# Performance work log

Hardware: AMD Instinct MI355X
Metric: run time of the kernel (lower is better)

The kernel has to match this reference:

```python
import jax, jax.numpy as jnp
import numpy as np


def squash(s, axis=-1):
    sq = jnp.sum(s * s, axis=axis, keepdims=True)
    return sq / (1.0 + sq) * s / (jnp.sqrt(sq) + 1e-8)


def setup_inputs() -> dict:
    key = jax.random.key(0)
    k1, k2 = jax.random.split(key)
    B, IN_CAPS, IN_DIM = 32, 2048, 16
    NUM_CAPS, CAPS_DIM = 32, 32
    x = jax.random.normal(k1, (B, IN_CAPS, IN_DIM), dtype=jnp.float32)
    W = 0.01 * jax.random.normal(k2, (NUM_CAPS, IN_CAPS, CAPS_DIM, IN_DIM), dtype=jnp.float32)
    return {"x": x, "W": W, "routing_steps": 3}


def reference(x, W, routing_steps):
    # u_hat[b, j, i, c] = W[j, i, c, d] @ x[b, i, d]
    u_hat = jnp.einsum('jicd,bid->bjic', W, x)
    du = jax.lax.stop_gradient(u_hat)  # routing uses detached predictions
    B, J, I, C = u_hat.shape
    b = jnp.zeros((B, J, I, 1), dtype=u_hat.dtype)
    for _ in range(routing_steps - 1):
        c = jax.nn.softmax(b, axis=1)                  # over output capsules j
        s = jnp.sum(c * du, axis=2)                    # [B, J, C]
        v = squash(s)
        b = b + jnp.einsum('bjic,bjc->bji', du, v)[..., None]
    c = jax.nn.softmax(b, axis=1)
    s = jnp.sum(c * u_hat, axis=2)
    v = squash(s)                                      # [B, J, C]
    return v
```

## Files before the change

### kernel.cpp

```cpp
#include <hip/hip_runtime.h>
#include <hip/hip_bf16.h>

#define B_SZ   32
#define I_CAPS 2048
#define J_CAPS 32
#define C_DIM  32
#define D_DIM  16

#define IT     8
#define TILES  8
#define SPLIT  32
#define MPAD   72

typedef _Float16 f16x8 __attribute__((ext_vector_type(8)));
typedef _Float16 f16x4 __attribute__((ext_vector_type(4)));
typedef float    f32x4 __attribute__((ext_vector_type(4)));

__device__ __forceinline__ float h2f_lo(unsigned int p) {
    union { unsigned short s; _Float16 h; } cv; cv.s = (unsigned short)(p & 0xffffu);
    return (float)cv.h;
}
__device__ __forceinline__ float h2f_hi(unsigned int p) { return h2f_lo(p >> 16); }


__global__ __launch_bounds__(256) void uhat_mfma(const float* __restrict__ W,
                                                 const float* __restrict__ x,
                                                 unsigned short* __restrict__ u) {
    const int t    = threadIdx.x;
    const int wave = t >> 6;
    const int lane = t & 63;
    const int lm   = lane & 15;
    const int lq   = lane >> 4;

    __shared__ unsigned short tr[4][32 * MPAD];
    unsigned short* my = tr[wave];

    const int i = blockIdx.x;

    f16x8 bfr[2];
#pragma unroll
    for (int nt = 0; nt < 2; ++nt) {
        const int b = nt * 16 + lm;
        const float4 xv = *reinterpret_cast<const float4*>(
            &x[((size_t)b * I_CAPS + i) * D_DIM + lq * 4]);
        f16x8 f = {};
        f[0] = (_Float16)xv.x; f[1] = (_Float16)xv.y;
        f[2] = (_Float16)xv.z; f[3] = (_Float16)xv.w;
        bfr[nt] = f;
    }

    float4 wv[16];
#pragma unroll
    for (int k = 0; k < 16; ++k) {
        const int mt = wave * 16 + k;
        const int j  = mt >> 1;
        const int c  = (mt & 1) * 16 + lm;
        wv[k] = *reinterpret_cast<const float4*>(
            &W[(((size_t)j * I_CAPS + i) * C_DIM + c) * D_DIM + lq * 4]);
    }

#pragma unroll
    for (int g = 0; g < 4; ++g) {
#pragma unroll
        for (int k4 = 0; k4 < 4; ++k4) {
            const int k = g * 4 + k4;
            f16x8 a = {};
            a[0] = (_Float16)wv[k].x; a[1] = (_Float16)wv[k].y;
            a[2] = (_Float16)wv[k].z; a[3] = (_Float16)wv[k].w;

            const f32x4 z = {0.f, 0.f, 0.f, 0.f};
            f32x4 d0 = __builtin_amdgcn_mfma_f32_16x16x32_f16(a, bfr[0], z, 0, 0, 0);
            f32x4 d1 = __builtin_amdgcn_mfma_f32_16x16x32_f16(a, bfr[1], z, 0, 0, 0);

            const int m_loc = k4 * 16 + lq * 4;
#pragma unroll
            for (int nt = 0; nt < 2; ++nt) {
                const f32x4 d = nt ? d1 : d0;
                f16x4 o;
                o[0] = (_Float16)d[0]; o[1] = (_Float16)d[1];
                o[2] = (_Float16)d[2]; o[3] = (_Float16)d[3];
                const int b = nt * 16 + lm;
                *reinterpret_cast<f16x4*>(&my[b * MPAD + m_loc]) = o;
            }
        }
        asm volatile("s_waitcnt lgkmcnt(0)" ::: "memory");
        __builtin_amdgcn_sched_barrier(0);

        const int b_off = lane >> 3;
        const int m_off = (lane & 7) * 8;
        const int m_base = wave * 256 + g * 64;
#pragma unroll
        for (int gb = 0; gb < 4; ++gb) {
            const int b = gb * 8 + b_off;
            const uint4 v = *reinterpret_cast<const uint4*>(&my[b * MPAD + m_off]);
            *reinterpret_cast<uint4*>(
                &u[((size_t)b * I_CAPS + i) * (J_CAPS * C_DIM) + m_base + m_off]) = v;
        }
    }
}

__global__ __launch_bounds__(256) void sum0_kernel(const unsigned short* __restrict__ u,
                                                   float* __restrict__ s0) {
    const int b      = blockIdx.x;
    const int i_base = blockIdx.y * (IT * TILES);
    const int t      = threadIdx.x;

    const uint2* u2 = reinterpret_cast<const uint2*>(u);
    float a0 = 0.f, a1 = 0.f, a2 = 0.f, a3 = 0.f;
#pragma unroll 8
    for (int ii = 0; ii < IT * TILES; ++ii) {
        const uint2 pk = u2[((size_t)b * I_CAPS + i_base + ii) * 256 + t];
        a0 += h2f_lo(pk.x); a1 += h2f_hi(pk.x);
        a2 += h2f_lo(pk.y); a3 += h2f_hi(pk.y);
    }
    const float sc = 1.0f / 32.0f;
    float* sp = &s0[(size_t)b * (J_CAPS * C_DIM) + t * 4];
    atomicAdd(sp + 0, a0 * sc);
    atomicAdd(sp + 1, a1 * sc);
    atomicAdd(sp + 2, a2 * sc);
    atomicAdd(sp + 3, a3 * sc);
}

__global__ __launch_bounds__(256) void route_pass(const unsigned short* __restrict__ u,
                                                  const float* __restrict__ s_prev,
                                                  float* __restrict__ V1,
                                                  float* __restrict__ s_out,
                                                  int pass) {
    const int isplit = blockIdx.x;
    const int b      = blockIdx.y;
    const int i_base = isplit * (IT * TILES);
    const int t      = threadIdx.x;

    __shared__ float Vs[J_CAPS * 33];
    __shared__ float cjs[IT * J_CAPS];

    const int jA = t & 31, iA = t >> 5;
    const int jB = t >> 3, c4 = (t & 7) * 4;

    {
        const size_t base = ((size_t)b * J_CAPS + jB) * C_DIM + c4;
        const float4 sv = *reinterpret_cast<const float4*>(&s_prev[base]);
        float sq = sv.x * sv.x + sv.y * sv.y + sv.z * sv.z + sv.w * sv.w;
#pragma unroll
        for (int msk = 4; msk >= 1; msk >>= 1) sq += __shfl_xor(sq, msk);
        const float scale = sq / ((1.f + sq) * (sqrtf(sq) + 1e-8f));
        float4 v;
        v.x = sv.x * scale; v.y = sv.y * scale;
        v.z = sv.z * scale; v.w = sv.w * scale;
        if (pass == 1 && isplit == 0)
            *reinterpret_cast<float4*>(&V1[base]) = v;
        if (pass == 2) {
            const float4 v1 = *reinterpret_cast<const float4*>(&V1[base]);
            v.x += v1.x; v.y += v1.y; v.z += v1.z; v.w += v1.w;
        }
        Vs[jB * 33 + c4 + 0] = v.x; Vs[jB * 33 + c4 + 1] = v.y;
        Vs[jB * 33 + c4 + 2] = v.z; Vs[jB * 33 + c4 + 3] = v.w;
    }
    __syncthreads();

    float sacc0 = 0.f, sacc1 = 0.f, sacc2 = 0.f, sacc3 = 0.f;

    const uint4* ub4 = reinterpret_cast<const uint4*>(
        u + (size_t)b * I_CAPS * (J_CAPS * C_DIM));
#define AROW(T) (ub4 + ((size_t)(i_base + (T) * IT + iA) * 128 + jA * 4))

    uint4 pa0, pa1, pa2, pa3, na0, na1, na2, na3;
    { const uint4* g = AROW(0); pa0 = g[0]; pa1 = g[1]; pa2 = g[2]; pa3 = g[3]; }

    const uint2* ub2 = reinterpret_cast<const uint2*>(
        u + (size_t)b * I_CAPS * (J_CAPS * C_DIM));

#pragma unroll
    for (int tile = 0; tile < TILES; ++tile) {
        {
            float l = 0.f;
#pragma unroll
            for (int q = 0; q < 4; ++q) {
                const uint4 pk = (q == 0) ? pa0 : (q == 1) ? pa1 : (q == 2) ? pa2 : pa3;
                const float* Vr = &Vs[jA * 33 + q * 8];
                l += h2f_lo(pk.x) * Vr[0] + h2f_hi(pk.x) * Vr[1]
                   + h2f_lo(pk.y) * Vr[2] + h2f_hi(pk.y) * Vr[3]
                   + h2f_lo(pk.z) * Vr[4] + h2f_hi(pk.z) * Vr[5]
                   + h2f_lo(pk.w) * Vr[6] + h2f_hi(pk.w) * Vr[7];
            }
            float m = l;
#pragma unroll
            for (int msk = 16; msk >= 1; msk >>= 1) m = fmaxf(m, __shfl_xor(m, msk));
            const float e = __expf(l - m);
            float ssum = e;
#pragma unroll
            for (int msk = 16; msk >= 1; msk >>= 1) ssum += __shfl_xor(ssum, msk);
            cjs[iA * J_CAPS + jA] = e / ssum;
        }
        __syncthreads();

        if (tile + 1 < TILES) {
            const uint4* g = AROW(tile + 1);
            na0 = g[0]; na1 = g[1]; na2 = g[2]; na3 = g[3];
        }

        {
            const int i0 = i_base + tile * IT;
#pragma unroll
            for (int il = 0; il < IT; ++il) {
                const float cj = cjs[il * J_CAPS + jB];
                const uint2 pk = ub2[(size_t)(i0 + il) * 256 + (jB * 8 + (t & 7))];
                sacc0 += cj * h2f_lo(pk.x);
                sacc1 += cj * h2f_hi(pk.x);
                sacc2 += cj * h2f_lo(pk.y);
                sacc3 += cj * h2f_hi(pk.y);
            }
        }
        __syncthreads();
        pa0 = na0; pa1 = na1; pa2 = na2; pa3 = na3;
    }
#undef AROW

    float* sp = &s_out[((size_t)b * J_CAPS + jB) * C_DIM + c4];
    atomicAdd(sp + 0, sacc0);
    atomicAdd(sp + 1, sacc1);
    atomicAdd(sp + 2, sacc2);
    atomicAdd(sp + 3, sacc3);
}

__global__ __launch_bounds__(256) void squash_out(const float* __restrict__ s,
                                                  float* __restrict__ out) {
    const int t   = threadIdx.x;
    const int row = blockIdx.x * 8 + (t >> 5);
    const int c   = t & 31;
    const float sv = s[row * 32 + c];
    float sq = sv * sv;
#pragma unroll
    for (int msk = 16; msk >= 1; msk >>= 1) sq += __shfl_xor(sq, msk);
    const float scale = sq / ((1.f + sq) * (sqrtf(sq) + 1e-8f));
    out[row * 32 + c] = sv * scale;
}

extern "C" void kernel_launch(void* const* d_in, const int* in_sizes, int n_in,
                              void* d_out, int out_size, void* d_ws, size_t ws_size,
                              hipStream_t stream) {
    const float* x = (const float*)d_in[0];
    const float* W = (const float*)d_in[1];
    float* out = (float*)d_out;

    const size_t u_elems = (size_t)B_SZ * I_CAPS * J_CAPS * C_DIM;
    const size_t sjc     = (size_t)B_SZ * J_CAPS * C_DIM;

    unsigned short* u = (unsigned short*)d_ws;
    float* s0 = (float*)((char*)d_ws + u_elems * 2);
    float* s1 = s0 + sjc;
    float* s2 = s1 + sjc;
    float* V1 = s2 + sjc;

    (void)hipMemsetAsync(s0, 0, 4 * sjc * sizeof(float), stream);

    uhat_mfma<<<I_CAPS, 256, 0, stream>>>(W, x, u);

    sum0_kernel<<<dim3(B_SZ, SPLIT), 256, 0, stream>>>(u, s0);
    route_pass<<<dim3(SPLIT, B_SZ), 256, 0, stream>>>(u, s0, V1, s1, 1);
    route_pass<<<dim3(SPLIT, B_SZ), 256, 0, stream>>>(u, s1, V1, s2, 2);

    squash_out<<<(B_SZ * J_CAPS * C_DIM) / 256, 256, 0, stream>>>(s2, out);
}
```

Before: 165.2 us.

## Restructure u_hat kernel grid to per-(j, i-chunk) blocks with smaller transpose tile

```diff
diff --git a/kernel.cpp b/kernel.cpp
--- a/kernel.cpp
+++ b/kernel.cpp
@@ -10,7 +10,7 @@
 #define IT     8
 #define TILES  8
 #define SPLIT  32
-#define MPAD   72
+#define TPAD   40
 
 typedef _Float16 f16x8 __attribute__((ext_vector_type(8)));
 typedef _Float16 f16x4 __attribute__((ext_vector_type(4)));
@@ -32,69 +32,69 @@
     const int lm   = lane & 15;
     const int lq   = lane >> 4;
 
-    __shared__ unsigned short tr[4][32 * MPAD];
+    __shared__ unsigned short tr[4][32 * TPAD];
     unsigned short* my = tr[wave];
 
-    const int i = blockIdx.x;
-
-    f16x8 bfr[2];
-#pragma unroll
-    for (int nt = 0; nt < 2; ++nt) {
-        const int b = nt * 16 + lm;
-        const float4 xv = *reinterpret_cast<const float4*>(
-            &x[((size_t)b * I_CAPS + i) * D_DIM + lq * 4]);
-        f16x8 f = {};
-        f[0] = (_Float16)xv.x; f[1] = (_Float16)xv.y;
-        f[2] = (_Float16)xv.z; f[3] = (_Float16)xv.w;
-        bfr[nt] = f;
-    }
-
-    float4 wv[16];
-#pragma unroll
-    for (int k = 0; k < 16; ++k) {
-        const int mt = wave * 16 + k;
-        const int j  = mt >> 1;
-        const int c  = (mt & 1) * 16 + lm;
-        wv[k] = *reinterpret_cast<const float4*>(
-            &W[(((size_t)j * I_CAPS + i) * C_DIM + c) * D_DIM + lq * 4]);
-    }
-
-#pragma unroll
-    for (int g = 0; g < 4; ++g) {
-#pragma unroll
-        for (int k4 = 0; k4 < 4; ++k4) {
-            const int k = g * 4 + k4;
-            f16x8 a = {};
-            a[0] = (_Float16)wv[k].x; a[1] = (_Float16)wv[k].y;
-            a[2] = (_Float16)wv[k].z; a[3] = (_Float16)wv[k].w;
-
-            const f32x4 z = {0.f, 0.f, 0.f, 0.f};
-            f32x4 d0 = __builtin_amdgcn_mfma_f32_16x16x32_f16(a, bfr[0], z, 0, 0, 0);
-            f32x4 d1 = __builtin_amdgcn_mfma_f32_16x16x32_f16(a, bfr[1], z, 0, 0, 0);
-
-            const int m_loc = k4 * 16 + lq * 4;
-#pragma unroll
-            for (int nt = 0; nt < 2; ++nt) {
-                const f32x4 d = nt ? d1 : d0;
-                f16x4 o;
-                o[0] = (_Float16)d[0]; o[1] = (_Float16)d[1];
-                o[2] = (_Float16)d[2]; o[3] = (_Float16)d[3];
-                const int b = nt * 16 + lm;
-                *reinterpret_cast<f16x4*>(&my[b * MPAD + m_loc]) = o;
-            }
-        }
+    const int j  = blockIdx.x;
+    const int i0 = blockIdx.y * 32 + wave * 8;
+
+    const int b_r = lane >> 2;
+    const int c_o = (lane & 3) * 8;
+
+    for (int ii = 0; ii < 8; ++ii) {
+        const int i = i0 + ii;
+
+        f16x8 bfr0 = {}, bfr1 = {};
+        {
+            const float4 xv0 = *reinterpret_cast<const float4*>(
+                &x[((size_t)lm * I_CAPS + i) * D_DIM + lq * 4]);
+            const float4 xv1 = *reinterpret_cast<const float4*>(
+                &x[((size_t)(16 + lm) * I_CAPS + i) * D_DIM + lq * 4]);
+            bfr0[0] = (_Float16)xv0.x; bfr0[1] = (_Float16)xv0.y;
+            bfr0[2] = (_Float16)xv0.z; bfr0[3] = (_Float16)xv0.w;
+            bfr1[0] = (_Float16)xv1.x; bfr1[1] = (_Float16)xv1.y;
+            bfr1[2] = (_Float16)xv1.z; bfr1[3] = (_Float16)xv1.w;
+        }
+
+        f16x8 a0 = {}, a1 = {};
+        {
+            const float* Wp = W + ((size_t)(j * I_CAPS + i) * C_DIM) * D_DIM;
+            const float4 w0 = *reinterpret_cast<const float4*>(
+                Wp + (lm * D_DIM) + lq * 4);
+            const float4 w1 = *reinterpret_cast<const float4*>(
+                Wp + ((16 + lm) * D_DIM) + lq * 4);
+            a0[0] = (_Float16)w0.x; a0[1] = (_Float16)w0.y;
+            a0[2] = (_Float16)w0.z; a0[3] = (_Float16)w0.w;
+            a1[0] = (_Float16)w1.x; a1[1] = (_Float16)w1.y;
+            a1[2] = (_Float16)w1.z; a1[3] = (_Float16)w1.w;
+        }
+
+        const f32x4 z = {0.f, 0.f, 0.f, 0.f};
+        f32x4 d00 = __builtin_amdgcn_mfma_f32_16x16x32_f16(a0, bfr0, z, 0, 0, 0);
+        f32x4 d01 = __builtin_amdgcn_mfma_f32_16x16x32_f16(a0, bfr1, z, 0, 0, 0);
+        f32x4 d10 = __builtin_amdgcn_mfma_f32_16x16x32_f16(a1, bfr0, z, 0, 0, 0);
+        f32x4 d11 = __builtin_amdgcn_mfma_f32_16x16x32_f16(a1, bfr1, z, 0, 0, 0);
+
+#define TWRITE(D, CT, NT)                                                       \
+        {                                                                       \
+            f16x4 o;                                                            \
+            o[0] = (_Float16)D[0]; o[1] = (_Float16)D[1];                       \
+            o[2] = (_Float16)D[2]; o[3] = (_Float16)D[3];                       \
+            *reinterpret_cast<f16x4*>(                                          \
+                &my[((NT) * 16 + lm) * TPAD + (CT) * 16 + lq * 4]) = o;         \
+        }
+        TWRITE(d00, 0, 0) TWRITE(d01, 0, 1) TWRITE(d10, 1, 0) TWRITE(d11, 1, 1)
+#undef TWRITE
+
         asm volatile("s_waitcnt lgkmcnt(0)" ::: "memory");
         __builtin_amdgcn_sched_barrier(0);
 
-        const int b_off = lane >> 3;
-        const int m_off = (lane & 7) * 8;
-        const int m_base = wave * 256 + g * 64;
-#pragma unroll
-        for (int gb = 0; gb < 4; ++gb) {
-            const int b = gb * 8 + b_off;
-            const uint4 v = *reinterpret_cast<const uint4*>(&my[b * MPAD + m_off]);
+#pragma unroll
+        for (int half = 0; half < 2; ++half) {
+            const int b = half * 16 + b_r;
+            const uint4 v = *reinterpret_cast<const uint4*>(&my[b * TPAD + c_o]);
             *reinterpret_cast<uint4*>(
-                &u[((size_t)b * I_CAPS + i) * (J_CAPS * C_DIM) + m_base + m_off]) = v;
+                &u[((size_t)b * I_CAPS + i) * (J_CAPS * C_DIM) + j * C_DIM + c_o]) = v;
         }
     }
 }
@@ -254,7 +254,7 @@
 
     (void)hipMemsetAsync(s0, 0, 4 * sjc * sizeof(float), stream);
 
-    uhat_mfma<<<I_CAPS, 256, 0, stream>>>(W, x, u);
+    uhat_mfma<<<dim3(J_CAPS, 64), 256, 0, stream>>>(W, x, u);
 
     sum0_kernel<<<dim3(B_SZ, SPLIT), 256, 0, stream>>>(u, s0);
     route_pass<<<dim3(SPLIT, B_SZ), 256, 0, stream>>>(u, s0, V1, s1, 1);
```

New measurement: 215.5 us. 1.3x slower.
